# Kernel tuning notes

Measured on AMD Instinct MI355X. Metric: run time of the kernel, lower is better.

The kernel has to match this reference:

```python
import jax, jax.numpy as jnp
import numpy as np

N = 30000   # nodes
E = 240000  # edges
G = 16      # graphs in batch
DIMS = [1, 256, 512, 1024]
OUT = 1024

def _xavier(key, fan_in, fan_out):
    lim = float(np.sqrt(6.0 / (fan_in + fan_out)))
    return jax.random.uniform(key, (fan_in, fan_out), minval=-lim, maxval=lim, dtype=jnp.float32)

def setup_inputs() -> dict:
    key = jax.random.key(0)
    ks = jax.random.split(key, 8)
    x = jax.random.normal(ks[0], (N, DIMS[0]), dtype=jnp.float32)
    edge_index = jax.random.randint(ks[1], (2, E), 0, N, dtype=jnp.int64)
    batch = jnp.sort(jax.random.randint(ks[2], (N,), 0, G, dtype=jnp.int64))
    W1 = _xavier(ks[3], DIMS[0], DIMS[1]); b1 = jnp.zeros((DIMS[1],), jnp.float32)
    W2 = _xavier(ks[4], DIMS[1], DIMS[2]); b2 = jnp.zeros((DIMS[2],), jnp.float32)
    W3 = _xavier(ks[5], DIMS[2], DIMS[3]); b3 = jnp.zeros((DIMS[3],), jnp.float32)
    Wo = _xavier(ks[6], DIMS[3], OUT);     bo = jnp.zeros((OUT,), jnp.float32)
    return {"x": x, "edge_index": edge_index, "batch": batch,
            "W1": W1, "b1": b1, "W2": W2, "b2": b2, "W3": W3, "b3": b3,
            "Wo": Wo, "bo": bo}

def reference(x, edge_index, batch, W1, b1, W2, b2, W3, b3, Wo, bo):
    n = x.shape[0]
    loops = jnp.arange(n)
    # GCNConv adds self-loops, then symmetric deg^-1/2 normalization
    src = jnp.concatenate([edge_index[0], loops])
    dst = jnp.concatenate([edge_index[1], loops])
    deg = jnp.zeros((n,), jnp.float32).at[dst].add(1.0)  # >=1 due to self-loops
    dis = jax.lax.rsqrt(deg)
    norm = (dis[src] * dis[dst])[:, None]  # [E+N, 1]

    def gcn(h, W, b):
        h = h @ W                                   # linear (no bias in lin)
        agg = jnp.zeros_like(h).at[dst].add(h[src] * norm)  # scatter-add messages
        return agg + b                              # GCNConv bias

    h = jax.nn.relu(gcn(x, W1, b1))
    h = jax.nn.relu(gcn(h, W2, b2))
    h = jax.nn.relu(gcn(h, W3, b3))
    # global mean pool over graphs
    sums = jnp.zeros((G, h.shape[1]), h.dtype).at[batch].add(h)
    cnt = jnp.zeros((G,), h.dtype).at[batch].add(1.0)
    pooled = sums / jnp.maximum(cnt, 1.0)[:, None]
    return pooled @ Wo + bo
```

## Files before the change

### kernel.cpp

```cpp
#include <hip/hip_runtime.h>
#include <hip/hip_bf16.h>
#include <stdint.h>

#define N_NODES 30000
#define E_EDGES 240000
#define NGRAPH  16
#define D1      256
#define D2      512
#define D3      1024
#define DOUT    1024
#define M_PAD   30720
#define NT_M    240
#define CAP     40

typedef unsigned short ushort_t;
typedef short short8 __attribute__((ext_vector_type(8)));
typedef float f32x4 __attribute__((ext_vector_type(4)));

__device__ __forceinline__ float bf2f(ushort_t u) {
    union { unsigned int i; float f; } v; v.i = ((unsigned int)u) << 16; return v.f;
}
__device__ __forceinline__ ushort_t f2bf(float x) {
    union { float f; unsigned int i; } v; v.f = x;
    unsigned int r = v.i + 0x7fffu + ((v.i >> 16) & 1u);
    return (ushort_t)(r >> 16);
}

__global__ void k_detect(const void* w1, const void* ei, int* flags) {
    int lane = threadIdx.x & 63;
    const ushort_t* h = (const ushort_t*)w1;
    float v = fabsf(bf2f(h[lane * 2]));
    unsigned long long badf = __ballot(!(v <= 0.25f));
    const int* e = (const int*)ei;
    unsigned long long badi = __ballot(e[lane * 2 + 1] != 0);
    if (threadIdx.x == 0) {
        flags[0] = (badf == 0ull) ? 1 : 0;
        flags[1] = (badi == 0ull) ? 1 : 0;
    }
}

__global__ void k_setup(const void* x, const void* batch, const void* w1, const void* b1,
                        const void* b2, const void* b3, const void* bo,
                        const void* W2, const void* W3,
                        float* xf, int* batch32, float* W1f, float* b1f, float* b2f,
                        float* b3f, float* bof, ushort_t* Wt2, ushort_t* Wt3,
                        int* slotcnt, float* pooled, float* pooled2, const int* flags) {
    int isbf = flags[0];
    int bid = blockIdx.x;
    int tid = threadIdx.x;
    if (bid < 492) {
        int i = bid * 256 + tid;
        if (i < 3072) {
            const void* src; float* dst; int idx;
            if      (i < 256)  { src = w1; dst = W1f; idx = i; }
            else if (i < 512)  { src = b1; dst = b1f; idx = i - 256; }
            else if (i < 1024) { src = b2; dst = b2f; idx = i - 512; }
            else if (i < 2048) { src = b3; dst = b3f; idx = i - 1024; }
            else               { src = bo; dst = bof; idx = i - 2048; }
            dst[idx] = isbf ? bf2f(((const ushort_t*)src)[idx]) : ((const float*)src)[idx];
        } else if (i < 33072) {
            int idx = i - 3072;
            xf[idx] = isbf ? bf2f(((const ushort_t*)x)[idx]) : ((const float*)x)[idx];
        } else if (i < 63072) {
            int idx = i - 33072;
            batch32[idx] = flags[1] ? (int)((const long long*)batch)[idx]
                                    : ((const int*)batch)[idx];
        } else if (i < 93072) {
            slotcnt[i - 63072] = 0;
        } else if (i < 109456) {
            pooled[i - 93072] = 0.0f;
        } else if (i < 125840) {
            pooled2[i - 109456] = 0.0f;
        }
    } else {
        __shared__ ushort_t tile[32][33];
        int tb = bid - 492;
        const void* in; ushort_t* out; int R, C, bx, by;
        if (tb < 128) { in = W2; out = Wt2; R = D1; C = D2; bx = tb & 15; by = tb >> 4; }
        else { tb -= 128; in = W3; out = Wt3; R = D2; C = D3; bx = tb & 31; by = tb >> 5; }
        int tx = tid & 31, ty = tid >> 5;
        int c0 = bx * 32, r0 = by * 32;
        for (int i = ty; i < 32; i += 8) {
            size_t idx = (size_t)(r0 + i) * C + c0 + tx;
            tile[i][tx] = isbf ? ((const ushort_t*)in)[idx] : f2bf(((const float*)in)[idx]);
        }
        __syncthreads();
        for (int i = ty; i < 32; i += 8) out[(size_t)(c0 + i) * R + r0 + tx] = tile[tx][i];
    }
}

__global__ void k_edge_count(const void* ei, int* slotcnt, int* slots, const int* flags) {
    int e = blockIdx.x * 256 + threadIdx.x;
    if (e >= E_EDGES) return;
    int s, d;
    if (flags[1]) {
        s = (int)((const long long*)ei)[e];
        d = (int)((const long long*)ei)[E_EDGES + e];
    } else {
        s = ((const int*)ei)[e];
        d = ((const int*)ei)[E_EDGES + e];
    }
    if ((unsigned)s >= N_NODES || (unsigned)d >= N_NODES) return;
    int pos = atomicAdd(&slotcnt[d], 1);
    if (pos < CAP) slots[d * CAP + pos] = s;
}

__global__ void k_s1(const float* xf, const int* slotcnt, const int* slots,
                     const int* batch, float* dis, float* s1, float* cntg) {
    int b = blockIdx.x;
    if (b == 118) {
        int g = threadIdx.x;
        if (g >= NGRAPH) return;
        int lo0 = 0, hi0 = N_NODES;
        while (lo0 < hi0) { int m = (lo0 + hi0) >> 1; if (batch[m] < g) lo0 = m + 1; else hi0 = m; }
        int lo1 = lo0, hi1 = N_NODES;
        while (lo1 < hi1) { int m = (lo1 + hi1) >> 1; if (batch[m] < g + 1) lo1 = m + 1; else hi1 = m; }
        cntg[g] = (float)(lo1 - lo0);
        return;
    }
    int d = b * 256 + threadIdx.x;
    if (d >= N_NODES) return;
    int cd = slotcnt[d];
    float di = rsqrtf(1.0f + (float)cd);
    dis[d] = di;
    int cnt = cd < CAP ? cd : CAP;
    float acc = xf[d] * di;
    for (int k = 0; k < cnt; k++) {
        int s = slots[d * CAP + k];
        acc += xf[s] * rsqrtf(1.0f + (float)slotcnt[s]);
    }
    s1[d] = acc * di;
}

__global__ void k_agg1(const float* s1, const float* W1f, const float* b1f,
                       ushort_t* a2, const int* slots, const int* slotcnt, const float* dis) {
    int node = blockIdx.x * 4 + (threadIdx.x >> 6);
    int lane = threadIdx.x & 63;
    int c4 = lane * 4;
    float w[4], bb[4], a[4];
    #pragma unroll
    for (int j = 0; j < 4; j++) { w[j] = W1f[c4 + j]; bb[j] = b1f[c4 + j]; }
    float di = dis[node];
    int cnt = slotcnt[node]; cnt = cnt < CAP ? cnt : CAP;
    float sv = s1[node];
    float wsl = di * di;
    #pragma unroll
    for (int j = 0; j < 4; j++) a[j] = wsl * fmaxf(sv * w[j] + bb[j], 0.0f);
    for (int k = 0; k < cnt; k++) {
        int s = slots[node * CAP + k];
        float ss = s1[s];
        float wn = dis[s] * di;
        #pragma unroll
        for (int j = 0; j < 4; j++) a[j] += wn * fmaxf(ss * w[j] + bb[j], 0.0f);
    }
    uint2 o;
    o.x = (unsigned int)f2bf(a[0]) | ((unsigned int)f2bf(a[1]) << 16);
    o.y = (unsigned int)f2bf(a[2]) | ((unsigned int)f2bf(a[3]) << 16);
    *(uint2*)&a2[(size_t)node * D1 + c4] = o;
}

__global__ void k_agg2(const ushort_t* h, ushort_t* out, const int* slots,
                       const int* slotcnt, const float* dis) {
    int node = blockIdx.x * 4 + (threadIdx.x >> 6);
    int lane = threadIdx.x & 63;
    int c8 = lane * 8;
    float di = dis[node];
    int cnt = slotcnt[node]; cnt = cnt < CAP ? cnt : CAP;
    float w = di * di;
    const ushort_t* hp = h + c8;
    short8 p = *(const short8*)&hp[(size_t)node * D2];
    float a[8];
    #pragma unroll
    for (int j = 0; j < 8; j++) a[j] = w * bf2f((ushort_t)p[j]);
    if (cnt > 0) {
        int s0 = slots[node * CAP];
        short8 q0 = *(const short8*)&hp[(size_t)s0 * D2];
        float ws0 = dis[s0] * di;
        for (int k = 1; k < cnt; k++) {
            int s1i = slots[node * CAP + k];
            short8 q1 = *(const short8*)&hp[(size_t)s1i * D2];
            float ws1 = dis[s1i] * di;
            #pragma unroll
            for (int j = 0; j < 8; j++) a[j] += ws0 * bf2f((ushort_t)q0[j]);
            q0 = q1; ws0 = ws1;
        }
        #pragma unroll
        for (int j = 0; j < 8; j++) a[j] += ws0 * bf2f((ushort_t)q0[j]);
    }
    uint4 o;
    o.x = (unsigned int)f2bf(a[0]) | ((unsigned int)f2bf(a[1]) << 16);
    o.y = (unsigned int)f2bf(a[2]) | ((unsigned int)f2bf(a[3]) << 16);
    o.z = (unsigned int)f2bf(a[4]) | ((unsigned int)f2bf(a[5]) << 16);
    o.w = (unsigned int)f2bf(a[6]) | ((unsigned int)f2bf(a[7]) << 16);
    *(uint4*)&out[(size_t)node * D2 + c8] = o;
}

__global__ __launch_bounds__(256, 3) void k_gemm(const ushort_t* A, const ushort_t* Bt,
                                                 const float* bias, ushort_t* Cmat,
                                                 int K, int Ncols, int ntn) {
    __shared__ __align__(16) ushort_t As[2][128 * 32];
    __shared__ __align__(16) ushort_t Bs[2][128 * 32];
    int tid = threadIdx.x;
    int id = blockIdx.x;
    int xcd = id & 7, q = id >> 3;
    int rt = xcd * (NT_M / 8) + q / ntn;
    int ct = q % ntn;
    int bm0 = rt * 128, bn0 = ct * 128;
    int wave = tid >> 6, lane = tid & 63;
    int wm = (wave & 1) * 64, wn = (wave >> 1) * 64;
    int l15 = lane & 15, quad = lane >> 4;

    int m1 = tid >> 2, k1 = (tid & 3) << 3;
    int m2 = m1 + 64;
    int off1 = m1 * 32 + k1, off2 = m2 * 32 + k1;
    const ushort_t* pA1 = A + (size_t)(bm0 + m1) * K + k1;
    const ushort_t* pA2 = A + (size_t)(bm0 + m2) * K + k1;
    const ushort_t* pB1 = Bt + (size_t)(bn0 + m1) * K + k1;
    const ushort_t* pB2 = Bt + (size_t)(bn0 + m2) * K + k1;

    {
        uint4 la0 = *(const uint4*)pA1, la1 = *(const uint4*)pA2;
        uint4 lb0 = *(const uint4*)pB1, lb1 = *(const uint4*)pB2;
        *(uint4*)&As[0][off1] = la0; *(uint4*)&As[0][off2] = la1;
        *(uint4*)&Bs[0][off1] = lb0; *(uint4*)&Bs[0][off2] = lb1;
    }

    f32x4 acc[4][4];
    for (int a = 0; a < 4; a++)
        for (int b = 0; b < 4; b++)
            acc[a][b] = (f32x4){0.f, 0.f, 0.f, 0.f};

    int niter = K >> 5;
    for (int it = 0; it < niter; ++it) {
        __syncthreads();
        int ktn = (it + 1) << 5;
        uint4 na0, na1, nb0, nb1;
        if (ktn < K) {
            na0 = *(const uint4*)(pA1 + ktn); na1 = *(const uint4*)(pA2 + ktn);
            nb0 = *(const uint4*)(pB1 + ktn); nb1 = *(const uint4*)(pB2 + ktn);
        }
        int cb = it & 1;
        short8 af[4], bfr[4];
        for (int im = 0; im < 4; im++)
            af[im] = *(const short8*)&As[cb][(wm + im * 16 + l15) * 32 + quad * 8];
        for (int in = 0; in < 4; in++)
            bfr[in] = *(const short8*)&Bs[cb][(wn + in * 16 + l15) * 32 + quad * 8];
        for (int im = 0; im < 4; im++)
            for (int in = 0; in < 4; in++)
                acc[im][in] = __builtin_amdgcn_mfma_f32_16x16x32_bf16(af[im], bfr[in], acc[im][in], 0, 0, 0);
        if (ktn < K) {
            int wb = cb ^ 1;
            *(uint4*)&As[wb][off1] = na0; *(uint4*)&As[wb][off2] = na1;
            *(uint4*)&Bs[wb][off1] = nb0; *(uint4*)&Bs[wb][off2] = nb1;
        }
    }

    for (int im = 0; im < 4; im++) {
        int row = bm0 + wm + im * 16 + quad * 4;
        for (int in = 0; in < 4; in++) {
            int col = bn0 + wn + in * 16 + l15;
            float bv = bias[col];
            for (int r = 0; r < 4; r++) {
                float v = acc[im][in][r] + bv;
                v = v > 0.0f ? v : 0.0f;
                Cmat[(size_t)(row + r) * Ncols + col] = f2bf(v);
            }
        }
    }
}

__global__ __launch_bounds__(256, 3) void k_gemm_pool(const ushort_t* A, const ushort_t* Bt,
                                                      const float* bias, const int* batch,
                                                      float* pooled, int K, int ntn) {
    __shared__ __align__(16) ushort_t As[2][128 * 32];
    __shared__ __align__(16) ushort_t Bs[2][128 * 32];
    int tid = threadIdx.x;
    int id = blockIdx.x;
    int xcd = id & 7, q = id >> 3;
    int rt = xcd * (NT_M / 8) + q / ntn;
    int ct = q % ntn;
    int bm0 = rt * 128, bn0 = ct * 128;
    int wave = tid >> 6, lane = tid & 63;
    int wm = (wave & 1) * 64, wn = (wave >> 1) * 64;
    int l15 = lane & 15, quad = lane >> 4;

    int m1 = tid >> 2, k1 = (tid & 3) << 3;
    int m2 = m1 + 64;
    int off1 = m1 * 32 + k1, off2 = m2 * 32 + k1;
    const ushort_t* pA1 = A + (size_t)(bm0 + m1) * K + k1;
    const ushort_t* pA2 = A + (size_t)(bm0 + m2) * K + k1;
    const ushort_t* pB1 = Bt + (size_t)(bn0 + m1) * K + k1;
    const ushort_t* pB2 = Bt + (size_t)(bn0 + m2) * K + k1;

    {
        uint4 la0 = *(const uint4*)pA1, la1 = *(const uint4*)pA2;
        uint4 lb0 = *(const uint4*)pB1, lb1 = *(const uint4*)pB2;
        *(uint4*)&As[0][off1] = la0; *(uint4*)&As[0][off2] = la1;
        *(uint4*)&Bs[0][off1] = lb0; *(uint4*)&Bs[0][off2] = lb1;
    }

    f32x4 acc[4][4];
    for (int a = 0; a < 4; a++)
        for (int b = 0; b < 4; b++)
            acc[a][b] = (f32x4){0.f, 0.f, 0.f, 0.f};

    int niter = K >> 5;
    for (int it = 0; it < niter; ++it) {
        __syncthreads();
        int ktn = (it + 1) << 5;
        uint4 na0, na1, nb0, nb1;
        if (ktn < K) {
            na0 = *(const uint4*)(pA1 + ktn); na1 = *(const uint4*)(pA2 + ktn);
            nb0 = *(const uint4*)(pB1 + ktn); nb1 = *(const uint4*)(pB2 + ktn);
        }
        int cb = it & 1;
        short8 af[4], bfr[4];
        for (int im = 0; im < 4; im++)
            af[im] = *(const short8*)&As[cb][(wm + im * 16 + l15) * 32 + quad * 8];
        for (int in = 0; in < 4; in++)
            bfr[in] = *(const short8*)&Bs[cb][(wn + in * 16 + l15) * 32 + quad * 8];
        for (int im = 0; im < 4; im++)
            for (int in = 0; in < 4; in++)
                acc[im][in] = __builtin_amdgcn_mfma_f32_16x16x32_bf16(af[im], bfr[in], acc[im][in], 0, 0, 0);
        if (ktn < K) {
            int wb = cb ^ 1;
            *(uint4*)&As[wb][off1] = na0; *(uint4*)&As[wb][off2] = na1;
            *(uint4*)&Bs[wb][off1] = nb0; *(uint4*)&Bs[wb][off2] = nb1;
        }
    }

    __syncthreads();
    float* pl = (float*)&As[0][0];
    int* gtile = (int*)&Bs[0][0];
    for (int i = tid; i < NGRAPH * 128; i += 256) pl[i] = 0.0f;
    if (tid < 128) {
        int r = bm0 + tid; if (r > N_NODES - 1) r = N_NODES - 1;
        int g = batch[r]; g = g < 0 ? 0 : (g > NGRAPH - 1 ? NGRAPH - 1 : g);
        gtile[tid] = g;
    }
    __syncthreads();

    int gmin = gtile[0], gmax = gtile[127];
    if (gmin == gmax && bm0 + 127 < N_NODES) {
        float csum[4];
        #pragma unroll
        for (int in = 0; in < 4; in++) csum[in] = 0.0f;
        for (int im = 0; im < 4; im++) {
            #pragma unroll
            for (int in = 0; in < 4; in++) {
                float bv = bias[bn0 + wn + in * 16 + l15];
                #pragma unroll
                for (int r = 0; r < 4; r++)
                    csum[in] += fmaxf(acc[im][in][r] + bv, 0.0f);
            }
        }
        #pragma unroll
        for (int in = 0; in < 4; in++) {
            csum[in] += __shfl_xor(csum[in], 16);
            csum[in] += __shfl_xor(csum[in], 32);
        }
        if (quad == 0) {
            #pragma unroll
            for (int in = 0; in < 4; in++)
                atomicAdd(&pl[gmin * 128 + wn + in * 16 + l15], csum[in]);
        }
    } else {
        for (int im = 0; im < 4; im++) {
            int rl = wm + im * 16 + quad * 4;
            for (int in = 0; in < 4; in++) {
                int cl = wn + in * 16 + l15;
                float bv = bias[bn0 + cl];
                float vsum = 0.0f;
                int gprev = gtile[rl];
                for (int r = 0; r < 4; r++) {
                    int row = bm0 + rl + r;
                    float v = (row < N_NODES) ? fmaxf(acc[im][in][r] + bv, 0.0f) : 0.0f;
                    int g = gtile[rl + r];
                    if (g != gprev) {
                        atomicAdd(&pl[gprev * 128 + cl], vsum);
                        vsum = 0.0f; gprev = g;
                    }
                    vsum += v;
                }
                atomicAdd(&pl[gprev * 128 + cl], vsum);
            }
        }
    }
    __syncthreads();

    int span = (gmax - gmin + 1) * 128;
    for (int idx = tid; idx < span; idx += 256) {
        int g = gmin + (idx >> 7), cl = idx & 127;
        float v = pl[g * 128 + cl];
        if (v != 0.0f) atomicAdd(&pooled[g * DOUT + bn0 + cl], v);
    }
}

__global__ __launch_bounds__(256) void k_out_partial(const float* pooled, const void* Wo,
                                                     float* pooled2, const int* flags) {
    __shared__ float pl[NGRAPH * 32];
    int tid = threadIdx.x;
    int col = blockIdx.x * 256 + tid;
    int k0 = blockIdx.y * 32;
    for (int i = tid; i < NGRAPH * 32; i += 256) {
        int g = i >> 5, kk = i & 31;
        pl[i] = pooled[g * D3 + k0 + kk];
    }
    __syncthreads();
    int isbf = flags[0];
    float acc[NGRAPH];
    #pragma unroll
    for (int g = 0; g < NGRAPH; g++) acc[g] = 0.0f;
    #pragma unroll 4
    for (int kk = 0; kk < 32; kk++) {
        int k = k0 + kk;
        float wv = isbf ? bf2f(((const ushort_t*)Wo)[(size_t)k * DOUT + col])
                        : ((const float*)Wo)[(size_t)k * DOUT + col];
        #pragma unroll
        for (int g = 0; g < NGRAPH; g++)
            acc[g] += pl[g * 32 + kk] * wv;
    }
    #pragma unroll
    for (int g = 0; g < NGRAPH; g++)
        atomicAdd(&pooled2[g * DOUT + col], acc[g]);
}

__global__ void k_out_fin(const float* pooled2, const float* bof, const float* cntg,
                          void* out, const int* flags) {
    int i = blockIdx.x * 256 + threadIdx.x;
    int g = i >> 10, o = i & 1023;
    float c = cntg[g]; c = c > 1.0f ? c : 1.0f;
    float v = pooled2[i] / c + bof[o];
    if (flags[0]) ((ushort_t*)out)[i] = f2bf(v);
    else          ((float*)out)[i] = v;
}

extern "C" void kernel_launch(void* const* d_in, const int* in_sizes, int n_in,
                              void* d_out, int out_size, void* d_ws, size_t ws_size,
                              hipStream_t stream) {
    const void* x_raw  = d_in[0];
    const void* ei_raw = d_in[1];
    const void* b_raw  = d_in[2];
    const void* W1_raw = d_in[3];
    const void* b1_raw = d_in[4];
    const void* W2_raw = d_in[5];
    const void* b2_raw = d_in[6];
    const void* W3_raw = d_in[7];
    const void* b3_raw = d_in[8];
    const void* Wo_raw = d_in[9];
    const void* bo_raw = d_in[10];

    char* w = (char*)d_ws;
    size_t off = 0;
    auto alloc = [&](size_t b) { size_t o = off; off += (b + 255) & ~(size_t)255; return o; };
    int*   flags   = (int*)  (w + alloc(256));
    float* xf      = (float*)(w + alloc((size_t)N_NODES * 4));
    int*   batch32 = (int*)  (w + alloc((size_t)N_NODES * 4));
    float* W1f     = (float*)(w + alloc(D1 * 4));
    float* b1f     = (float*)(w + alloc(D1 * 4));
    float* b2f     = (float*)(w + alloc(D2 * 4));
    float* b3f     = (float*)(w + alloc(D3 * 4));
    float* bof     = (float*)(w + alloc(DOUT * 4));
    float* dis     = (float*)(w + alloc((size_t)N_NODES * 4));
    float* s1      = (float*)(w + alloc((size_t)N_NODES * 4));
    float* cntg    = (float*)(w + alloc(64));
    float* pooled  = (float*)(w + alloc((size_t)NGRAPH * DOUT * 4));
    float* pooled2 = (float*)(w + alloc((size_t)NGRAPH * DOUT * 4));
    int*   slotcnt = (int*)  (w + alloc((size_t)N_NODES * 4));
    int*   slots   = (int*)  (w + alloc((size_t)N_NODES * CAP * 4));
    ushort_t* Wt2  = (ushort_t*)(w + alloc((size_t)D2 * D1 * 2));
    ushort_t* Wt3  = (ushort_t*)(w + alloc((size_t)D3 * D2 * 2));
    ushort_t* slabA = (ushort_t*)(w + alloc((size_t)M_PAD * D2 * 2));
    ushort_t* a2 = slabA;
    ushort_t* a3 = slabA;
    ushort_t* h2   = (ushort_t*)(w + alloc((size_t)M_PAD * D2 * 2));

    int nb_e = (E_EDGES + 255) / 256;

    k_detect<<<1, 64, 0, stream>>>(W1_raw, ei_raw, flags);
    k_setup<<<1132, 256, 0, stream>>>(x_raw, b_raw, W1_raw, b1_raw, b2_raw, b3_raw, bo_raw,
                                      W2_raw, W3_raw, xf, batch32, W1f, b1f, b2f, b3f, bof,
                                      Wt2, Wt3, slotcnt, pooled, pooled2, flags);
    k_edge_count<<<nb_e, 256, 0, stream>>>(ei_raw, slotcnt, slots, flags);
    k_s1<<<119, 256, 0, stream>>>(xf, slotcnt, slots, batch32, dis, s1, cntg);

    k_agg1<<<N_NODES / 4, 256, 0, stream>>>(s1, W1f, b1f, a2, slots, slotcnt, dis);
    k_gemm<<<NT_M * (D2 / 128), 256, 0, stream>>>(a2, Wt2, b2f, h2, D1, D2, D2 / 128);
    k_agg2<<<N_NODES / 4, 256, 0, stream>>>(h2, a3, slots, slotcnt, dis);
    k_gemm_pool<<<NT_M * (D3 / 128), 256, 0, stream>>>(a3, Wt3, b3f, batch32, pooled, D2, D3 / 128);

    k_out_partial<<<dim3(DOUT / 256, D3 / 32), 256, 0, stream>>>(pooled, Wo_raw, pooled2, flags);
    k_out_fin<<<NGRAPH * DOUT / 256, 256, 0, stream>>>(pooled2, bof, cntg, d_out, flags);
}
```

Baseline: 245.1 us.

## Inline dtype detection, transpose neighbor slot layout, deepen gather prefetch

Removes the separate k_detect launch by having each kernel detect the input dtypes inline with a wavefront ballot. The neighbor slot table moves from node-major to slot-major layout so per-thread reads in k_s1 coalesce across nodes. The gather loops in k_agg1 and k_agg2 now keep two neighbors in flight instead of one. In exchange, every kernel repeats the small detection load, and the slot-major layout spreads the scattered writes in k_edge_count across memory.

New measurement: 252.3 us. 1.03x slower.

```diff
diff --git a/kernel.cpp b/kernel.cpp
--- a/kernel.cpp
+++ b/kernel.cpp
@@ -26,26 +26,24 @@
     return (ushort_t)(r >> 16);
 }
 
-__global__ void k_detect(const void* w1, const void* ei, int* flags) {
+__device__ __forceinline__ int detect_isbf(const void* w1) {
     int lane = threadIdx.x & 63;
-    const ushort_t* h = (const ushort_t*)w1;
-    float v = fabsf(bf2f(h[lane * 2]));
-    unsigned long long badf = __ballot(!(v <= 0.25f));
-    const int* e = (const int*)ei;
-    unsigned long long badi = __ballot(e[lane * 2 + 1] != 0);
-    if (threadIdx.x == 0) {
-        flags[0] = (badf == 0ull) ? 1 : 0;
-        flags[1] = (badi == 0ull) ? 1 : 0;
-    }
+    float v = fabsf(bf2f(((const ushort_t*)w1)[lane * 2]));
+    return __ballot(!(v <= 0.25f)) == 0ull;
+}
+__device__ __forceinline__ int detect_isi64(const void* ei) {
+    int lane = threadIdx.x & 63;
+    return __ballot(((const int*)ei)[lane * 2 + 1] != 0) == 0ull;
 }
 
 __global__ void k_setup(const void* x, const void* batch, const void* w1, const void* b1,
                         const void* b2, const void* b3, const void* bo,
-                        const void* W2, const void* W3,
+                        const void* W2, const void* W3, const void* ei,
                         float* xf, int* batch32, float* W1f, float* b1f, float* b2f,
                         float* b3f, float* bof, ushort_t* Wt2, ushort_t* Wt3,
-                        int* slotcnt, float* pooled, float* pooled2, const int* flags) {
-    int isbf = flags[0];
+                        int* slotcnt, float* pooled, float* pooled2) {
+    int isbf = detect_isbf(w1);
+    int isi64 = detect_isi64(ei);
     int bid = blockIdx.x;
     int tid = threadIdx.x;
     if (bid < 492) {
@@ -63,8 +61,8 @@
             xf[idx] = isbf ? bf2f(((const ushort_t*)x)[idx]) : ((const float*)x)[idx];
         } else if (i < 63072) {
             int idx = i - 33072;
-            batch32[idx] = flags[1] ? (int)((const long long*)batch)[idx]
-                                    : ((const int*)batch)[idx];
+            batch32[idx] = isi64 ? (int)((const long long*)batch)[idx]
+                                 : ((const int*)batch)[idx];
         } else if (i < 93072) {
             slotcnt[i - 63072] = 0;
         } else if (i < 109456) {
@@ -89,11 +87,12 @@
     }
 }
 
-__global__ void k_edge_count(const void* ei, int* slotcnt, int* slots, const int* flags) {
+__global__ void k_edge_count(const void* ei, int* slotcnt, int* slots) {
+    int isi64 = detect_isi64(ei);
     int e = blockIdx.x * 256 + threadIdx.x;
     if (e >= E_EDGES) return;
     int s, d;
-    if (flags[1]) {
+    if (isi64) {
         s = (int)((const long long*)ei)[e];
         d = (int)((const long long*)ei)[E_EDGES + e];
     } else {
@@ -102,7 +101,7 @@
     }
     if ((unsigned)s >= N_NODES || (unsigned)d >= N_NODES) return;
     int pos = atomicAdd(&slotcnt[d], 1);
-    if (pos < CAP) slots[d * CAP + pos] = s;
+    if (pos < CAP) slots[pos * N_NODES + d] = s;
 }
 
 __global__ void k_s1(const float* xf, const int* slotcnt, const int* slots,
@@ -126,7 +125,7 @@
     int cnt = cd < CAP ? cd : CAP;
     float acc = xf[d] * di;
     for (int k = 0; k < cnt; k++) {
-        int s = slots[d * CAP + k];
+        int s = slots[k * N_NODES + d];
         acc += xf[s] * rsqrtf(1.0f + (float)slotcnt[s]);
     }
     s1[d] = acc * di;
@@ -146,12 +145,27 @@
     float wsl = di * di;
     #pragma unroll
     for (int j = 0; j < 4; j++) a[j] = wsl * fmaxf(sv * w[j] + bb[j], 0.0f);
-    for (int k = 0; k < cnt; k++) {
-        int s = slots[node * CAP + k];
-        float ss = s1[s];
-        float wn = dis[s] * di;
-        #pragma unroll
-        for (int j = 0; j < 4; j++) a[j] += wn * fmaxf(ss * w[j] + bb[j], 0.0f);
+    if (cnt > 0) {
+        int sA = slots[node];
+        float vA = s1[sA], wA = dis[sA] * di;
+        if (cnt > 1) {
+            int sB = slots[N_NODES + node];
+            float vB = s1[sB], wB = dis[sB] * di;
+            for (int k = 2; k < cnt; k++) {
+                int sC = slots[k * N_NODES + node];
+                float vC = s1[sC], wC = dis[sC] * di;
+                #pragma unroll
+                for (int j = 0; j < 4; j++) a[j] += wA * fmaxf(vA * w[j] + bb[j], 0.0f);
+                vA = vB; wA = wB; vB = vC; wB = wC;
+            }
+            #pragma unroll
+            for (int j = 0; j < 4; j++) a[j] += wA * fmaxf(vA * w[j] + bb[j], 0.0f);
+            #pragma unroll
+            for (int j = 0; j < 4; j++) a[j] += wB * fmaxf(vB * w[j] + bb[j], 0.0f);
+        } else {
+            #pragma unroll
+            for (int j = 0; j < 4; j++) a[j] += wA * fmaxf(vA * w[j] + bb[j], 0.0f);
+        }
     }
     uint2 o;
     o.x = (unsigned int)f2bf(a[0]) | ((unsigned int)f2bf(a[1]) << 16);
@@ -173,19 +187,29 @@
     #pragma unroll
     for (int j = 0; j < 8; j++) a[j] = w * bf2f((ushort_t)p[j]);
     if (cnt > 0) {
-        int s0 = slots[node * CAP];
-        short8 q0 = *(const short8*)&hp[(size_t)s0 * D2];
-        float ws0 = dis[s0] * di;
-        for (int k = 1; k < cnt; k++) {
-            int s1i = slots[node * CAP + k];
-            short8 q1 = *(const short8*)&hp[(size_t)s1i * D2];
-            float ws1 = dis[s1i] * di;
-            #pragma unroll
-            for (int j = 0; j < 8; j++) a[j] += ws0 * bf2f((ushort_t)q0[j]);
-            q0 = q1; ws0 = ws1;
-        }
-        #pragma unroll
-        for (int j = 0; j < 8; j++) a[j] += ws0 * bf2f((ushort_t)q0[j]);
+        int sA = slots[node];
+        short8 qA = *(const short8*)&hp[(size_t)sA * D2];
+        float wA = dis[sA] * di;
+        if (cnt > 1) {
+            int sB = slots[N_NODES + node];
+            short8 qB = *(const short8*)&hp[(size_t)sB * D2];
+            float wB = dis[sB] * di;
+            for (int k = 2; k < cnt; k++) {
+                int sC = slots[k * N_NODES + node];
+                short8 qC = *(const short8*)&hp[(size_t)sC * D2];
+                float wC = dis[sC] * di;
+                #pragma unroll
+                for (int j = 0; j < 8; j++) a[j] += wA * bf2f((ushort_t)qA[j]);
+                qA = qB; wA = wB; qB = qC; wB = wC;
+            }
+            #pragma unroll
+            for (int j = 0; j < 8; j++) a[j] += wA * bf2f((ushort_t)qA[j]);
+            #pragma unroll
+            for (int j = 0; j < 8; j++) a[j] += wB * bf2f((ushort_t)qB[j]);
+        } else {
+            #pragma unroll
+            for (int j = 0; j < 8; j++) a[j] += wA * bf2f((ushort_t)qA[j]);
+        }
     }
     uint4 o;
     o.x = (unsigned int)f2bf(a[0]) | ((unsigned int)f2bf(a[1]) << 16);
@@ -397,7 +421,8 @@
 }
 
 __global__ __launch_bounds__(256) void k_out_partial(const float* pooled, const void* Wo,
-                                                     float* pooled2, const int* flags) {
+                                                     float* pooled2, const void* w1) {
+    int isbf = detect_isbf(w1);
     __shared__ float pl[NGRAPH * 32];
     int tid = threadIdx.x;
     int col = blockIdx.x * 256 + tid;
@@ -407,7 +432,6 @@
         pl[i] = pooled[g * D3 + k0 + kk];
     }
     __syncthreads();
-    int isbf = flags[0];
     float acc[NGRAPH];
     #pragma unroll
     for (int g = 0; g < NGRAPH; g++) acc[g] = 0.0f;
@@ -426,13 +450,14 @@
 }
 
 __global__ void k_out_fin(const float* pooled2, const float* bof, const float* cntg,
-                          void* out, const int* flags) {
+                          void* out, const void* w1) {
+    int isbf = detect_isbf(w1);
     int i = blockIdx.x * 256 + threadIdx.x;
     int g = i >> 10, o = i & 1023;
     float c = cntg[g]; c = c > 1.0f ? c : 1.0f;
     float v = pooled2[i] / c + bof[o];
-    if (flags[0]) ((ushort_t*)out)[i] = f2bf(v);
-    else          ((float*)out)[i] = v;
+    if (isbf) ((ushort_t*)out)[i] = f2bf(v);
+    else      ((float*)out)[i] = v;
 }
 
 extern "C" void kernel_launch(void* const* d_in, const int* in_sizes, int n_in,
@@ -453,7 +478,6 @@
     char* w = (char*)d_ws;
     size_t off = 0;
     auto alloc = [&](size_t b) { size_t o = off; off += (b + 255) & ~(size_t)255; return o; };
-    int*   flags   = (int*)  (w + alloc(256));
     float* xf      = (float*)(w + alloc((size_t)N_NODES * 4));
     int*   batch32 = (int*)  (w + alloc((size_t)N_NODES * 4));
     float* W1f     = (float*)(w + alloc(D1 * 4));
@@ -477,11 +501,10 @@
 
     int nb_e = (E_EDGES + 255) / 256;
 
-    k_detect<<<1, 64, 0, stream>>>(W1_raw, ei_raw, flags);
     k_setup<<<1132, 256, 0, stream>>>(x_raw, b_raw, W1_raw, b1_raw, b2_raw, b3_raw, bo_raw,
-                                      W2_raw, W3_raw, xf, batch32, W1f, b1f, b2f, b3f, bof,
-                                      Wt2, Wt3, slotcnt, pooled, pooled2, flags);
-    k_edge_count<<<nb_e, 256, 0, stream>>>(ei_raw, slotcnt, slots, flags);
+                                      W2_raw, W3_raw, ei_raw, xf, batch32, W1f, b1f, b2f,
+                                      b3f, bof, Wt2, Wt3, slotcnt, pooled, pooled2);
+    k_edge_count<<<nb_e, 256, 0, stream>>>(ei_raw, slotcnt, slots);
     k_s1<<<119, 256, 0, stream>>>(xf, slotcnt, slots, batch32, dis, s1, cntg);
 
     k_agg1<<<N_NODES / 4, 256, 0, stream>>>(s1, W1f, b1f, a2, slots, slotcnt, dis);
@@ -489,6 +512,6 @@
     k_agg2<<<N_NODES / 4, 256, 0, stream>>>(h2, a3, slots, slotcnt, dis);
     k_gemm_pool<<<NT_M * (D3 / 128), 256, 0, stream>>>(a3, Wt3, b3f, batch32, pooled, D2, D3 / 128);
 
-    k_out_partial<<<dim3(DOUT / 256, D3 / 32), 256, 0, stream>>>(pooled, Wo_raw, pooled2, flags);
-    k_out_fin<<<NGRAPH * DOUT / 256, 256, 0, stream>>>(pooled2, bof, cntg, d_out, flags);
-}
+    k_out_partial<<<dim3(DOUT / 256, D3 / 32), 256, 0, stream>>>(pooled, Wo_raw, pooled2, W1_raw);
+    k_out_fin<<<NGRAPH * DOUT / 256, 256, 0, stream>>>(pooled2, bof, cntg, d_out, W1_raw);
+}
```
